# Performance work log

Measured on AMD Instinct MI355X. Metric: run time of the kernel, lower is better.

The kernel has to match this reference:

```python
import jax, jax.numpy as jnp
import numpy as np

N = 512       # num_nodes (feature dim of x == num_nodes, per GCNConv(num_nodes, f1))
BZ = 32       # subjects
TC = 256      # tc_length
F1 = 256
F2 = 128
E = 524288    # edges in the given (corr) graph over all bz*N nodes
NTOT = BZ * N
SLOPE = 0.2   # leaky relu negative_slope


def setup_inputs() -> dict:
    key = jax.random.key(0)
    ks = jax.random.split(key, 17)
    w = lambda k, shape: (jax.random.normal(k, shape, jnp.float32) * (shape[-1] ** -0.5))
    return {
        "x": jax.random.normal(ks[0], (NTOT, N), jnp.float32),
        "t": jax.random.normal(ks[1], (NTOT, TC), jnp.float32),
        "gumbel_u": jax.random.uniform(ks[2], (BZ, N, N, 2), jnp.float32),
        "edge_index": jax.random.randint(ks[3], (2, E), 0, NTOT, jnp.int64 if jax.config.jax_enable_x64 else jnp.int32),
        "conv1_w": w(ks[4], (F1, N)),
        "conv1_b": jnp.zeros((F1,), jnp.float32),
        "conv2_w": w(ks[5], (F2, F1)),
        "conv2_b": jnp.zeros((F2,), jnp.float32),
        "fc_cat_w": w(ks[6], (2, 2 * TC)),
        "fc_cat_b": jnp.zeros((2,), jnp.float32),
        "fcn1_w": w(ks[7], (256, F2 * 2 * N)),
        "fcn1_b": jnp.zeros((256,), jnp.float32),
        "fcn2_w": w(ks[8], (32, 256)),
        "fcn2_b": jnp.zeros((32,), jnp.float32),
        "fcn3_w": w(ks[9], (2, 32)),
        "fcn3_b": jnp.zeros((2,), jnp.float32),
    }


def _gcn_dense(x, A, W, b):
    # PyG GCNConv on a dense 0/1 adjacency A (edge r->c means A[r,c]=1):
    # add self loop, in-degree symmetric norm, aggregate sources into targets.
    n = A.shape[0]
    Ah = A + jnp.eye(n, dtype=A.dtype)
    deg = Ah.sum(axis=0)                                  # in-degree (targets = cols)
    dis = jnp.where(deg > 0, jax.lax.rsqrt(deg), 0.0)
    M = dis[:, None] * Ah * dis[None, :]                  # M[j,i] = d_j^-1/2 A_hat[j,i] d_i^-1/2
    return M.T @ (x @ W.T) + b


def _gcn_sparse(x, row, col, W, b):
    n = x.shape[0]
    loops = jnp.arange(n, dtype=row.dtype)
    r = jnp.concatenate([row, loops])
    c = jnp.concatenate([col, loops])
    deg = jax.ops.segment_sum(jnp.ones_like(c, x.dtype), c, num_segments=n)
    dis = jnp.where(deg > 0, jax.lax.rsqrt(deg), 0.0)
    norm = dis[r] * dis[c]                                # [E+n]
    xw = x @ W.T                                          # [n, out]
    out = jax.ops.segment_sum(xw[r] * norm[:, None], c, num_segments=n)
    return out + b


def reference(x, t, gumbel_u, edge_index, conv1_w, conv1_b, conv2_w, conv2_b,
              fc_cat_w, fc_cat_b, fcn1_w, fcn1_b, fcn2_w, fcn2_b, fcn3_w, fcn3_b):
    bz = t.shape[0] // N
    tb = t.reshape(bz, N, -1)
    xb = x.reshape(bz, N, -1)
    # fc_cat(relu(cat([senders, receivers]))) factors into per-node terms:
    Ws = fc_cat_w[:, :TC]   # multiplies senders half
    Wr = fc_cat_w[:, TC:]   # multiplies receivers half

    def per_sample(ti, xi, ui):
        u = jax.nn.relu(ti)                               # [N, TC]
        ls = u @ Ws.T                                     # [N, 2] sender term
        lr = u @ Wr.T                                     # [N, 2] receiver term
        # pair k = i*N+j has receiver t_i, sender t_j
        logits = lr[:, None, :] + ls[None, :, :] + fc_cat_b   # [N, N, 2]
        g = -jnp.log(-jnp.log(jnp.clip(ui, 1e-9, 1.0 - 1e-9)))  # Gumbel(0,1)
        y = logits + g                                    # tau = 1
        A = (jnp.argmax(y, axis=-1) == 0).astype(xi.dtype)    # hard sample, class 0 => edge
        A = jax.lax.stop_gradient(A)                      # torch.where -> indices blocks grad
        h = jax.nn.relu(_gcn_dense(xi, A, conv1_w, conv1_b))
        return _gcn_dense(h, A, conv2_w, conv2_b)         # [N, F2]

    x_op = jax.vmap(per_sample)(tb, xb, gumbel_u)         # [bz, N, F2]

    row, col = edge_index[0], edge_index[1]
    x_corr = jax.nn.relu(_gcn_sparse(x, row, col, conv1_w, conv1_b))
    x_corr = _gcn_sparse(x_corr, row, col, conv2_w, conv2_b)   # [bz*N, F2]

    emb = jnp.concatenate([x_op.reshape(-1, F2), x_corr], axis=1)  # [bz*N, 2*F2]
    emb = emb.reshape(bz, -1)                             # [bz, 2*F2*N]
    h = jax.nn.leaky_relu(emb @ fcn1_w.T + fcn1_b, SLOPE)
    h = jax.nn.leaky_relu(h @ fcn2_w.T + fcn2_b, SLOPE)
    return h @ fcn3_w.T + fcn3_b                          # [bz, 2]
```

## Files before the change

kernel.cpp:

```cpp
#include <hip/hip_runtime.h>
#include <hip/hip_bf16.h>

typedef __bf16 bf16_t;
typedef __bf16 bf16x8 __attribute__((ext_vector_type(8)));
typedef __bf16 bf16x4 __attribute__((ext_vector_type(4)));
typedef float f32x4 __attribute__((ext_vector_type(4)));

constexpr int kN = 512;
constexpr int kBZ = 32;
constexpr int kTC = 256;
constexpr int kE = 524288;
constexpr int kNTOT = 16384;

__device__ __forceinline__ void gll16(const bf16_t* g, bf16_t* l) {
    __builtin_amdgcn_global_load_lds((const __attribute__((address_space(1))) void*)g,
                                     (__attribute__((address_space(3))) void*)l, 16, 0, 0);
}

template <int NI>
__device__ __forceinline__ void stageT(const bf16_t* __restrict__ src, int ld,
                                       bf16_t* lds, int wave, int lane) {
#pragma unroll
    for (int i = 0; i < NI; i++) {
        int r0 = (wave * NI + i) * 8;
        int r = r0 + (lane >> 3);
        int c = (lane & 7) ^ (r & 7);
        gll16(src + (size_t)r * ld + c * 8, lds + r0 * 64);
    }
}

__device__ __forceinline__ bf16x8 rdfrag(const bf16_t* lds, int row, int cc) {
    return *(const bf16x8*)(lds + row * 64 + ((cc ^ (row & 7)) * 8));
}

__global__ __launch_bounds__(256) void k_front(const float* __restrict__ c1w, const float* __restrict__ c2w,
                                               bf16_t* __restrict__ c1b, bf16_t* __restrict__ c2b,
                                               int* __restrict__ counts, float* __restrict__ degsum,
                                               const float* __restrict__ tin, const float* __restrict__ fcw,
                                               const float* __restrict__ fcb, float4* __restrict__ lsr) {
    int b = blockIdx.x;
    if (b < 192) {
        int i = b * 256 + threadIdx.x;
        const int n0 = 32768, n1 = n0 + 8192, n2 = n1 + 4096, n3 = n2 + 4096;
        if (i < n0) {
            float4 v = ((const float4*)c1w)[i];
            bf16x4 o = {(bf16_t)v.x, (bf16_t)v.y, (bf16_t)v.z, (bf16_t)v.w};
            ((bf16x4*)c1b)[i] = o;
        } else if (i < n1) {
            int j = i - n0;
            float4 v = ((const float4*)c2w)[j];
            bf16x4 o = {(bf16_t)v.x, (bf16_t)v.y, (bf16_t)v.z, (bf16_t)v.w};
            ((bf16x4*)c2b)[j] = o;
        } else if (i < n2) {
            ((int4*)counts)[i - n1] = make_int4(0, 0, 0, 0);
        } else if (i < n3) {
            ((float4*)degsum)[i - n2] = make_float4(0.f, 0.f, 0.f, 0.f);
        }
    } else {
        int row = (b - 192) * 4 + (threadIdx.x >> 6);
        int lane = threadIdx.x & 63;
        const float* tr = tin + (size_t)row * kTC;
        float s0 = 0, s1 = 0, r0 = 0, r1 = 0;
        for (int k = lane; k < kTC; k += 64) {
            float u = fmaxf(tr[k], 0.f);
            s0 += u * fcw[k];
            s1 += u * fcw[512 + k];
            r0 += u * fcw[256 + k];
            r1 += u * fcw[768 + k];
        }
#pragma unroll
        for (int off = 32; off > 0; off >>= 1) {
            s0 += __shfl_down(s0, off); s1 += __shfl_down(s1, off);
            r0 += __shfl_down(r0, off); r1 += __shfl_down(r1, off);
        }
        if (lane == 0) lsr[row] = make_float4(s0 + fcb[0], s1 + fcb[1], r0, r1);
    }
}

__global__ __launch_bounds__(256) void k_adjhist(const float* __restrict__ gum, const float4* __restrict__ lsr,
                                                 bf16_t* __restrict__ AT, float* __restrict__ degsum,
                                                 const int* __restrict__ col, int* __restrict__ counts) {
    int blk = blockIdx.x;
    if (blk >= 2048) {
        int e = (blk - 2048) * 256 + threadIdx.x;
        if (e < kE) atomicAdd(&counts[col[e]], 1);
        return;
    }
    int s = blk >> 6;
    int a0 = ((blk >> 3) & 7) * 64, b0 = (blk & 7) * 64;
    __shared__ bf16_t tile[64][72];
    int t = threadIdx.x;
    int lb = t & 63, ra = t >> 6;
    int b = b0 + lb;
    float4 pb = lsr[s * kN + b];
#pragma unroll 4
    for (int p = 0; p < 16; p++) {
        int a = a0 + p * 4 + ra;
        float4 qa = lsr[s * kN + a];
        float2 gv = *(const float2*)(gum + ((((size_t)s * kN + a) * kN + b) << 1));
        float u0 = fmaxf(gv.x, 1e-9f);
        float u1 = fmaxf(gv.y, 1e-9f);
        float g0 = -__logf(-__logf(u0));
        float g1 = -__logf(-__logf(u1));
        float v = ((qa.z + pb.x + g0) >= (qa.w + pb.y + g1)) ? 1.f : 0.f;
        if (a == b) v += 1.f;
        tile[lb][p * 4 + ra] = (bf16_t)v;
    }
    __syncthreads();
    int rj = t >> 3, li = (t & 7) * 8;
#pragma unroll
    for (int p = 0; p < 2; p++) {
        int j = p * 32 + rj;
        bf16x8 v = *(const bf16x8*)&tile[j][li];
        *(bf16x8*)(AT + ((size_t)s * kN + b0 + j) * kN + a0 + li) = v;
        float ps = 0;
#pragma unroll
        for (int q = 0; q < 8; q++) ps += (float)v[q];
        ps += __shfl_down(ps, 4);
        ps += __shfl_down(ps, 2);
        ps += __shfl_down(ps, 1);
        if ((t & 7) == 0) atomicAdd(degsum + s * kN + b0 + j, ps);
    }
}

template <int MODE, int GDEC>
__global__ __launch_bounds__(256) void k_gemm(const bf16_t* __restrict__ A, const bf16_t* __restrict__ B,
                                              bf16_t* __restrict__ C, int K, int lda, int ldb, int ldc,
                                              size_t sA, size_t sB, size_t sC,
                                              const float* __restrict__ degsum, const float* __restrict__ bias) {
    int m0, n0, s;
    {
        int f = blockIdx.x;
        s = ((f >> 5) << 3) | (f & 7);
        m0 = ((f >> 3) & 3) * 128;
        n0 = 0;
    }
    const bf16_t* Ab = A + sA * s + (size_t)m0 * lda;
    const bf16_t* Bb = B + sB * s + (size_t)n0 * ldb;
    C += sC * s;
    __shared__ __align__(16) bf16_t As[2][128 * 64], Bs[2][128 * 64];
    f32x4 acc[4][4] = {};
    int tid = threadIdx.x;
    int wave = tid >> 6, lane = tid & 63;
    int wm = (wave & 1) * 64, wn = (wave >> 1) * 64;
    int fm = lane & 15, fq = lane >> 4;
    stageT<4>(Ab, lda, As[0], wave, lane);
    stageT<4>(Bb, ldb, Bs[0], wave, lane);
    int cur = 0;
    for (int kb = 0;;) {
        int kn = kb + 64;
        __syncthreads();
        if (kn < K) {
            stageT<4>(Ab + kn, lda, As[cur ^ 1], wave, lane);
            stageT<4>(Bb + kn, ldb, Bs[cur ^ 1], wave, lane);
        }
#pragma unroll
        for (int kk = 0; kk < 2; kk++) {
            bf16x8 af[4], bfr[4];
#pragma unroll
            for (int i = 0; i < 4; i++) {
                af[i] = rdfrag(As[cur], wm + i * 16 + fm, kk * 4 + fq);
                bfr[i] = rdfrag(Bs[cur], wn + i * 16 + fm, kk * 4 + fq);
            }
#pragma unroll
            for (int i = 0; i < 4; i++)
#pragma unroll
                for (int j = 0; j < 4; j++)
                    acc[i][j] = __builtin_amdgcn_mfma_f32_16x16x32_bf16(af[i], bfr[j], acc[i][j], 0, 0, 0);
        }
        kb = kn;
        if (kb >= K) break;
        cur ^= 1;
    }
#pragma unroll
    for (int i = 0; i < 4; i++) {
#pragma unroll
        for (int r = 0; r < 4; r++) {
            int row = wm + i * 16 + fq * 4 + r;
            float sc = rsqrtf(degsum[(size_t)s * kN + m0 + row]);
#pragma unroll
            for (int j = 0; j < 4; j++) {
                int col = n0 + wn + j * 16 + fm;
                float v = sc * acc[i][j][r] + bias[col];
                if constexpr (MODE == 1) v = fmaxf(v, 0.f);
                C[(size_t)(m0 + row) * ldc + col] = (bf16_t)v;
            }
        }
    }
}

__global__ __launch_bounds__(256) void k_gcn1f(const bf16_t* __restrict__ AT, const bf16_t* __restrict__ Z1T,
                                               const bf16_t* __restrict__ C2W, const float* __restrict__ degsum,
                                               const float* __restrict__ c1b, bf16_t* __restrict__ Z2T) {
    int f = blockIdx.x;
    int s = ((f >> 6) << 3) | (f & 7);
    int mt = (f >> 3) & 7;
    const bf16_t* Ab = AT + (size_t)s * (512 * 512) + (size_t)(mt * 64) * 512;
    const bf16_t* Bb = Z1T + (size_t)s * (256 * 512);
    __shared__ __align__(16) bf16_t smem[40960];
    bf16_t* Hs = smem;
    int tid = threadIdx.x, wave = tid >> 6, lane = tid & 63;
    int fm = lane & 15, fq = lane >> 4;
    f32x4 acc[4][4] = {};
    stageT<2>(Ab, 512, smem, wave, lane);
    stageT<8>(Bb, 512, smem + 8192, wave, lane);
    int cur = 0;
    for (int kb = 0;;) {
        int kn = kb + 64;
        bf16_t* Ac = cur ? smem + 4096 : smem;
        bf16_t* An = cur ? smem : smem + 4096;
        bf16_t* Bc = cur ? smem + 24576 : smem + 8192;
        bf16_t* Bn = cur ? smem + 8192 : smem + 24576;
        __syncthreads();
        if (kn < 512) {
            stageT<2>(Ab + kn, 512, An, wave, lane);
            stageT<8>(Bb + kn, 512, Bn, wave, lane);
        }
        int wn = wave * 64;
#pragma unroll
        for (int kk = 0; kk < 2; kk++) {
            bf16x8 af[4], bfr[4];
#pragma unroll
            for (int i = 0; i < 4; i++) {
                af[i] = rdfrag(Ac, i * 16 + fm, kk * 4 + fq);
                bfr[i] = rdfrag(Bc, wn + i * 16 + fm, kk * 4 + fq);
            }
#pragma unroll
            for (int i = 0; i < 4; i++)
#pragma unroll
                for (int j = 0; j < 4; j++)
                    acc[i][j] = __builtin_amdgcn_mfma_f32_16x16x32_bf16(af[i], bfr[j], acc[i][j], 0, 0, 0);
        }
        kb = kn;
        if (kb >= 512) break;
        cur ^= 1;
    }
    __syncthreads();
    stageT<4>(C2W, 256, smem + 16384, wave, lane);
    {
        int wn = wave * 64;
#pragma unroll
        for (int i = 0; i < 4; i++) {
#pragma unroll
            for (int r = 0; r < 4; r++) {
                int row = i * 16 + fq * 4 + r;
                float sc = rsqrtf(degsum[(size_t)s * 512 + mt * 64 + row]);
#pragma unroll
                for (int j = 0; j < 4; j++) {
                    int col = wn + j * 16 + fm;
                    float v = fmaxf(sc * acc[i][j][r] + c1b[col], 0.f);
                    int c = col >> 3;
                    int cS = (c & 24) | ((c & 7) ^ (row & 7));
                    Hs[row * 256 + cS * 8 + (col & 7)] = (bf16_t)v;
                }
            }
        }
    }
    f32x4 acc2[4][2] = {};
    int cur2 = 0;
    for (int kb2 = 0;;) {
        int kn2 = kb2 + 64;
        bf16_t* B2c = cur2 ? smem + 24576 : smem + 16384;
        bf16_t* B2n = cur2 ? smem + 16384 : smem + 24576;
        __syncthreads();
        if (kn2 < 256) stageT<4>(C2W + kn2, 256, B2n, wave, lane);
        int wc = wave * 32;
#pragma unroll
        for (int kk = 0; kk < 2; kk++) {
            int cbase = (kb2 >> 3) + kk * 4 + fq;
            bf16x8 af2[4], bfr2[2];
#pragma unroll
            for (int i = 0; i < 4; i++) {
                int row = i * 16 + fm;
                int cS = (cbase & 24) | ((cbase & 7) ^ (row & 7));
                af2[i] = *(const bf16x8*)&Hs[row * 256 + cS * 8];
            }
#pragma unroll
            for (int j = 0; j < 2; j++) bfr2[j] = rdfrag(B2c, wc + j * 16 + fm, kk * 4 + fq);
#pragma unroll
            for (int i = 0; i < 4; i++)
#pragma unroll
                for (int j = 0; j < 2; j++)
                    acc2[i][j] = __builtin_amdgcn_mfma_f32_16x16x32_bf16(af2[i], bfr2[j], acc2[i][j], 0, 0, 0);
        }
        kb2 = kn2;
        if (kb2 >= 256) break;
        cur2 ^= 1;
    }
    __syncthreads();
    {
        int wc = wave * 32;
#pragma unroll
        for (int i = 0; i < 4; i++) {
#pragma unroll
            for (int r = 0; r < 4; r++) {
                int row = i * 16 + fq * 4 + r;
                float sc = rsqrtf(degsum[(size_t)s * 512 + mt * 64 + row]);
#pragma unroll
                for (int j = 0; j < 2; j++) {
                    int fcol = wc + j * 16 + fm;
                    smem[fcol * 72 + row] = (bf16_t)(sc * acc2[i][j][r]);
                }
            }
        }
    }
    __syncthreads();
    {
        int fr = tid >> 1, half = tid & 1;
        bf16_t* zp = Z2T + ((size_t)(s * 128 + fr)) * 512 + mt * 64 + half * 32;
        const bf16_t* tp = &smem[fr * 72 + half * 32];
#pragma unroll
        for (int q = 0; q < 4; q++) *(bf16x8*)(zp + q * 8) = *(const bf16x8*)(tp + q * 8);
    }
}

template <bool AF32, int F, int DENSE_ROWS, bool PAIRXY>
__global__ __launch_bounds__(256) void k_gemmT(const void* __restrict__ Ap, const bf16_t* __restrict__ B,
                                               bf16_t* __restrict__ XW, bf16_t* __restrict__ ZT, int K,
                                               const float* __restrict__ degsum) {
    int m0, n0;
    if constexpr (PAIRXY) {
        int f = blockIdx.x;
        m0 = (((f >> 4) << 3) | (f & 7)) * 128;
        n0 = ((f >> 3) & 1) * 128;
    } else {
        m0 = blockIdx.x * 128;
        n0 = blockIdx.y * 128;
    }
    constexpr int AST = AF32 ? 9216 : 8192;
    __shared__ __align__(16) bf16_t smem[2 * AST + 2 * 8192];
    bf16_t* A0 = smem;
    bf16_t* A1 = smem + AST;
    bf16_t* B0 = smem + 2 * AST;
    bf16_t* B1 = smem + 2 * AST + 8192;
    f32x4 acc[4][4] = {};
    int tid = threadIdx.x;
    int wave = tid >> 6, lane = tid & 63;
    int wm = (wave & 1) * 64, wn = (wave >> 1) * 64;
    int fm = lane & 15, fq = lane >> 4;
    int srow = tid >> 3, scol = (tid & 7) * 8;
    const float* Af = (const float*)Ap;
    const bf16_t* Abf = (const bf16_t*)Ap;
    if constexpr (AF32) {
#pragma unroll
        for (int p = 0; p < 4; p++) {
            int row = p * 32 + srow;
            const float* ap = Af + (size_t)(m0 + row) * K + scol;
            float4 lo = *(const float4*)ap, hi = *(const float4*)(ap + 4);
            bf16x8 o = {(bf16_t)lo.x, (bf16_t)lo.y, (bf16_t)lo.z, (bf16_t)lo.w,
                        (bf16_t)hi.x, (bf16_t)hi.y, (bf16_t)hi.z, (bf16_t)hi.w};
            *(bf16x8*)&A0[row * 72 + scol] = o;
        }
    } else {
        stageT<4>(Abf + (size_t)m0 * K, K, A0, wave, lane);
    }
    stageT<4>(B + (size_t)n0 * K, K, B0, wave, lane);
    int cur = 0;
    for (int kb = 0;;) {
        int kn = kb + 64;
        bool more = kn < K;
        bf16_t* Ac = cur ? A1 : A0;
        bf16_t* An = cur ? A0 : A1;
        bf16_t* Bc = cur ? B1 : B0;
        bf16_t* Bn = cur ? B0 : B1;
        float4 plo[4], phi[4];
        __syncthreads();
        if (more) {
            if constexpr (AF32) {
#pragma unroll
                for (int p = 0; p < 4; p++) {
                    int row = p * 32 + srow;
                    const float* ap = Af + (size_t)(m0 + row) * K + kn + scol;
                    plo[p] = *(const float4*)ap;
                    phi[p] = *(const float4*)(ap + 4);
                }
            } else {
                stageT<4>(Abf + (size_t)m0 * K + kn, K, An, wave, lane);
            }
            stageT<4>(B + (size_t)n0 * K + kn, K, Bn, wave, lane);
        }
#pragma unroll
        for (int kk = 0; kk < 2; kk++) {
            bf16x8 af[4], bfr[4];
#pragma unroll
            for (int i = 0; i < 4; i++) {
                if constexpr (AF32)
                    af[i] = *(const bf16x8*)&Ac[(wm + i * 16 + fm) * 72 + kk * 32 + fq * 8];
                else
                    af[i] = rdfrag(Ac, wm + i * 16 + fm, kk * 4 + fq);
                bfr[i] = rdfrag(Bc, wn + i * 16 + fm, kk * 4 + fq);
            }
#pragma unroll
            for (int i = 0; i < 4; i++)
#pragma unroll
                for (int j = 0; j < 4; j++)
                    acc[i][j] = __builtin_amdgcn_mfma_f32_16x16x32_bf16(af[i], bfr[j], acc[i][j], 0, 0, 0);
        }
        if constexpr (AF32) {
            if (more) {
#pragma unroll
                for (int p = 0; p < 4; p++) {
                    int row = p * 32 + srow;
                    bf16x8 o = {(bf16_t)plo[p].x, (bf16_t)plo[p].y, (bf16_t)plo[p].z, (bf16_t)plo[p].w,
                                (bf16_t)phi[p].x, (bf16_t)phi[p].y, (bf16_t)phi[p].z, (bf16_t)phi[p].w};
                    *(bf16x8*)&An[row * 72 + scol] = o;
                }
            }
        }
        kb = kn;
        if (kb >= K) break;
        cur ^= 1;
    }
    bool doT = (m0 < DENSE_ROWS);
    __syncthreads();
#pragma unroll
    for (int i = 0; i < 4; i++) {
#pragma unroll
        for (int r = 0; r < 4; r++) {
            int row = wm + i * 16 + fq * 4 + r;
            float sc = doT ? rsqrtf(degsum[m0 + row]) : 0.f;
#pragma unroll
            for (int j = 0; j < 4; j++) {
                int col = wn + j * 16 + fm;
                float v = acc[i][j][r];
                XW[(size_t)(m0 + row) * F + n0 + col] = (bf16_t)v;
                if (doT) smem[col * 136 + row] = (bf16_t)(sc * v);
            }
        }
    }
    if (doT) {
        __syncthreads();
        int fr = tid >> 1, hi = (tid & 1) * 64;
        bf16_t* zrow = ZT + ((size_t)(m0 >> 9) * F + n0 + fr) * kN + (m0 & 511) + hi;
#pragma unroll
        for (int q = 0; q < 8; q++)
            *(bf16x8*)(zrow + q * 8) = *(const bf16x8*)&smem[fr * 136 + hi + q * 8];
    }
}


__global__ __launch_bounds__(1024) void k_scan(const int* __restrict__ counts, int* __restrict__ offsets,
                                               int* __restrict__ cursor, float* __restrict__ dis_s) {
    __shared__ int ldc_[16896];
    __shared__ int sums[1024];
    int t = threadIdx.x;
#define IDX(j) ((j) + ((j) >> 5))
    for (int i = 0; i < 16; i++) {
        int g = i * 1024 + t;
        int c = counts[g];
        ldc_[IDX(g)] = c;
        dis_s[g] = rsqrtf((float)(c + 1));
    }
    __syncthreads();
    int s = 0;
    for (int i = 0; i < 16; i++) s += ldc_[IDX(t * 16 + i)];
    sums[t] = s;
    __syncthreads();
    for (int off = 1; off < 1024; off <<= 1) {
        int y = (t >= off) ? sums[t - off] : 0;
        __syncthreads();
        sums[t] += y;
        __syncthreads();
    }
    int run = sums[t] - s;
    for (int i = 0; i < 16; i++) {
        int j = t * 16 + i;
        int c = ldc_[IDX(j)];
        ldc_[IDX(j)] = run;
        run += c;
    }
    __syncthreads();
    for (int i = 0; i < 16; i++) {
        int g = i * 1024 + t;
        int o = ldc_[IDX(g)];
        offsets[g] = o;
        cursor[g] = o;
    }
#undef IDX
}

__global__ __launch_bounds__(256) void k_fill(const int* __restrict__ row, const int* __restrict__ col,
                                              int* __restrict__ cursor, int* __restrict__ list) {
    int e = blockIdx.x * 256 + threadIdx.x;
    if (e < kE) {
        int p = atomicAdd(&cursor[col[e]], 1);
        list[p] = row[e];
    }
}

template <int F, bool RELU>
__global__ __launch_bounds__(256) void k_sagg(const bf16_t* __restrict__ XW, int rowOffIn,
                                              const int* __restrict__ list, const int* __restrict__ offsets,
                                              const int* __restrict__ counts, const float* __restrict__ dis_s,
                                              const float* __restrict__ bias, bf16_t* __restrict__ OUT,
                                              int outColOff) {
    constexpr int TPR = F / 8;
    constexpr int RPB = 256 / TPR;
    int j = blockIdx.x * RPB + threadIdx.x / TPR;
    int f8 = (threadIdx.x % TPR) * 8;
    float dj = dis_s[j];
    const bf16_t* base = XW + (size_t)rowOffIn * F;
    float acc[8];
    {
        bf16x8 v = *(const bf16x8*)(base + (size_t)j * F + f8);
#pragma unroll
        for (int q = 0; q < 8; q++) acc[q] = dj * (float)v[q];
    }
    int off = offsets[j], cnt = counts[j];
    int e = 0;
    int nb = cnt & ~7;
    if (nb) {
        int r[8];
#pragma unroll
        for (int q = 0; q < 8; q++) r[q] = list[off + q];
        while (true) {
            int en = e + 8;
            bool more = en < nb;
            int rn[8];
            if (more) {
#pragma unroll
                for (int q = 0; q < 8; q++) rn[q] = list[off + en + q];
            }
            float d[8];
#pragma unroll
            for (int q = 0; q < 8; q++) d[q] = dis_s[r[q]];
            bf16x8 v0 = *(const bf16x8*)(base + (size_t)r[0] * F + f8);
            bf16x8 v1 = *(const bf16x8*)(base + (size_t)r[1] * F + f8);
            bf16x8 v2 = *(const bf16x8*)(base + (size_t)r[2] * F + f8);
            bf16x8 v3 = *(const bf16x8*)(base + (size_t)r[3] * F + f8);
            bf16x8 v4 = *(const bf16x8*)(base + (size_t)r[4] * F + f8);
            bf16x8 v5 = *(const bf16x8*)(base + (size_t)r[5] * F + f8);
            bf16x8 v6 = *(const bf16x8*)(base + (size_t)r[6] * F + f8);
            bf16x8 v7 = *(const bf16x8*)(base + (size_t)r[7] * F + f8);
#pragma unroll
            for (int q = 0; q < 8; q++)
                acc[q] += ((d[0] * (float)v0[q] + d[1] * (float)v1[q]) + (d[2] * (float)v2[q] + d[3] * (float)v3[q])) +
                          ((d[4] * (float)v4[q] + d[5] * (float)v5[q]) + (d[6] * (float)v6[q] + d[7] * (float)v7[q]));
            e = en;
            if (!more) break;
#pragma unroll
            for (int q = 0; q < 8; q++) r[q] = rn[q];
        }
    }
    for (; e + 4 <= cnt; e += 4) {
        int r0 = list[off + e], r1 = list[off + e + 1], r2 = list[off + e + 2], r3 = list[off + e + 3];
        float d0 = dis_s[r0], d1 = dis_s[r1], d2 = dis_s[r2], d3 = dis_s[r3];
        bf16x8 v0 = *(const bf16x8*)(base + (size_t)r0 * F + f8);
        bf16x8 v1 = *(const bf16x8*)(base + (size_t)r1 * F + f8);
        bf16x8 v2 = *(const bf16x8*)(base + (size_t)r2 * F + f8);
        bf16x8 v3 = *(const bf16x8*)(base + (size_t)r3 * F + f8);
#pragma unroll
        for (int q = 0; q < 8; q++)
            acc[q] += (d0 * (float)v0[q] + d1 * (float)v1[q]) + (d2 * (float)v2[q] + d3 * (float)v3[q]);
    }
    for (; e < cnt; e++) {
        int r = list[off + e];
        float d = dis_s[r];
        bf16x8 v = *(const bf16x8*)(base + (size_t)r * F + f8);
#pragma unroll
        for (int q = 0; q < 8; q++) acc[q] += d * (float)v[q];
    }
    bf16x8 o;
#pragma unroll
    for (int q = 0; q < 8; q++) {
        float v = dj * acc[q] + bias[f8 + q];
        if (RELU) v = fmaxf(v, 0.f);
        o[q] = (bf16_t)v;
    }
    *(bf16x8*)(OUT + (size_t)j * 256 + outColOff + f8) = o;
}

__global__ __launch_bounds__(256) void k_fcn1(const bf16_t* __restrict__ EMB, const float* __restrict__ W1,
                                              float* __restrict__ partials) {
    int tid = threadIdx.x, wave = tid >> 6, lane = tid & 63;
    int fm = lane & 15, fq = lane >> 4;
    int kb0 = blockIdx.x * 512;
    f32x4 acc[2][4] = {};
#pragma unroll 4
    for (int ks = 0; ks < 512; ks += 32) {
        int k = kb0 + ks + fq * 8;
        bf16x8 a0 = *(const bf16x8*)(EMB + (size_t)fm * 131072 + k);
        bf16x8 a1 = *(const bf16x8*)(EMB + (size_t)(16 + fm) * 131072 + k);
        bf16x8 bfr[4];
#pragma unroll
        for (int j = 0; j < 4; j++) {
            int n = wave * 64 + j * 16 + fm;
            const float* p = W1 + (size_t)n * 131072 + k;
            float4 lo = *(const float4*)p;
            float4 hi = *(const float4*)(p + 4);
            bf16x8 b = {(bf16_t)lo.x, (bf16_t)lo.y, (bf16_t)lo.z, (bf16_t)lo.w,
                        (bf16_t)hi.x, (bf16_t)hi.y, (bf16_t)hi.z, (bf16_t)hi.w};
            bfr[j] = b;
        }
#pragma unroll
        for (int j = 0; j < 4; j++) {
            acc[0][j] = __builtin_amdgcn_mfma_f32_16x16x32_bf16(a0, bfr[j], acc[0][j], 0, 0, 0);
            acc[1][j] = __builtin_amdgcn_mfma_f32_16x16x32_bf16(a1, bfr[j], acc[1][j], 0, 0, 0);
        }
    }
    float* P = partials + (size_t)blockIdx.x * 8192;
#pragma unroll
    for (int i = 0; i < 2; i++)
#pragma unroll
        for (int j = 0; j < 4; j++)
#pragma unroll
            for (int r = 0; r < 4; r++)
                P[(size_t)(i * 16 + fq * 4 + r) * 256 + wave * 64 + j * 16 + fm] = acc[i][j][r];
}

__global__ __launch_bounds__(256) void k_reduce(const float* __restrict__ partials, float* __restrict__ h1pre) {
    __shared__ float red[8][32];
    int t = threadIdx.x;
    int el = t & 31, q = t >> 5;
    int e = blockIdx.x * 32 + el;
    float s = 0;
#pragma unroll 8
    for (int i = 0; i < 32; i++) s += partials[(size_t)(q * 32 + i) * 8192 + e];
    red[q][el] = s;
    __syncthreads();
    if (t < 32) {
        float r = 0;
#pragma unroll
        for (int qq = 0; qq < 8; qq++) r += red[qq][t];
        h1pre[blockIdx.x * 32 + t] = r;
    }
}

__global__ __launch_bounds__(256) void k_head(const float* __restrict__ h1pre, const float* __restrict__ b1,
                                              const float* __restrict__ W2, const float* __restrict__ b2,
                                              const float* __restrict__ W3, const float* __restrict__ b3,
                                              float* __restrict__ out) {
    __shared__ float h1s[32][256];
    __shared__ float h2s[32][32];
    int t = threadIdx.x;
    for (int i = 0; i < 32; i++) {
        float s = h1pre[i * 256 + t] + b1[t];
        h1s[i][t] = (s > 0.f) ? s : 0.2f * s;
    }
    __syncthreads();
    for (int p = 0; p < 4; p++) {
        int id = p * 256 + t, si = id >> 5, o2 = id & 31;
        float s = 0;
        for (int k = 0; k < 256; k++) s += h1s[si][k] * W2[o2 * 256 + k];
        s += b2[o2];
        h2s[si][o2] = (s > 0.f) ? s : 0.2f * s;
    }
    __syncthreads();
    if (t < 64) {
        int si = t >> 1, o3 = t & 1;
        float s = 0;
#pragma unroll
        for (int k = 0; k < 32; k++) s += h2s[si][k] * W3[o3 * 32 + k];
        out[si * 2 + o3] = s + b3[o3];
    }
}


extern "C" void kernel_launch(void* const* d_in, const int* in_sizes, int n_in,
                              void* d_out, int out_size, void* d_ws, size_t ws_size,
                              hipStream_t stream) {
    const float* x = (const float*)d_in[0];
    const float* t = (const float*)d_in[1];
    const float* gum = (const float*)d_in[2];
    const int* eidx = (const int*)d_in[3];
    const float* c1w = (const float*)d_in[4];
    const float* c1b = (const float*)d_in[5];
    const float* c2w = (const float*)d_in[6];
    const float* c2b = (const float*)d_in[7];
    const float* fcw = (const float*)d_in[8];
    const float* fcb = (const float*)d_in[9];
    const float* w1 = (const float*)d_in[10];
    const float* b1 = (const float*)d_in[11];
    const float* w2 = (const float*)d_in[12];
    const float* b2 = (const float*)d_in[13];
    const float* w3 = (const float*)d_in[14];
    const float* b3 = (const float*)d_in[15];
    float* out = (float*)d_out;
    (void)in_sizes; (void)n_in; (void)out_size; (void)ws_size;

    char* ws = (char*)d_ws;
    size_t off = 0;
    auto alloc = [&](size_t bytes) -> char* {
        char* p = ws + off;
        off += (bytes + 255) & ~size_t(255);
        return p;
    };
    bf16_t* c1wb = (bf16_t*)alloc((size_t)256 * 512 * 2);
    bf16_t* c2wb = (bf16_t*)alloc((size_t)128 * 256 * 2);
    float4* lsr = (float4*)alloc((size_t)kNTOT * 16);
    bf16_t* AT = (bf16_t*)alloc((size_t)kBZ * kN * kN * 2);
    float* degsum = (float*)alloc((size_t)kNTOT * 4);
    bf16_t* XW1_EMB = (bf16_t*)alloc((size_t)kNTOT * 256 * 2);
    bf16_t* Z1T = (bf16_t*)alloc((size_t)kBZ * 256 * 512 * 2);
    bf16_t* H = (bf16_t*)alloc((size_t)32768 * 256 * 2);
    bf16_t* XW2 = (bf16_t*)alloc((size_t)32768 * 128 * 2);
    bf16_t* Z2T = (bf16_t*)alloc((size_t)kBZ * 128 * 512 * 2);
    int* counts = (int*)alloc((size_t)kNTOT * 4);
    int* offsets = (int*)alloc((size_t)kNTOT * 4);
    int* cursor = (int*)alloc((size_t)kNTOT * 4);
    float* diss = (float*)alloc((size_t)kNTOT * 4);
    int* list = (int*)alloc((size_t)kE * 4);
    float* partials = (float*)alloc((size_t)256 * 8192 * 4);
    float* h1pre = (float*)alloc((size_t)8192 * 4);

    bf16_t* XW1 = XW1_EMB;
    bf16_t* EMB = XW1_EMB;

    k_front<<<4288, 256, 0, stream>>>(c1w, c2w, c1wb, c2wb, counts, degsum, t, fcw, fcb, lsr);
    k_adjhist<<<4096, 256, 0, stream>>>(gum, lsr, AT, degsum, eidx + kE, counts);
    k_scan<<<1, 1024, 0, stream>>>(counts, offsets, cursor, diss);
    k_fill<<<2048, 256, 0, stream>>>(eidx, eidx + kE, cursor, list);
    k_gemmT<true, 256, kNTOT, true><<<256, 256, 0, stream>>>(x, c1wb, XW1, Z1T, 512, degsum);
    k_gcn1f<<<256, 256, 0, stream>>>(AT, Z1T, c2wb, degsum, c1b, Z2T);
    k_sagg<256, true><<<2048, 256, 0, stream>>>(XW1, 0, list, offsets, counts, diss, c1b,
                                                H + (size_t)16384 * 256, 0);
    k_gemmT<false, 128, 0, false><<<dim3(128, 1, 1), 256, 0, stream>>>(H + (size_t)16384 * 256, c2wb,
                                                                       XW2 + (size_t)16384 * 128, Z2T, 256, degsum);
    k_gemm<2, 2><<<128, 256, 0, stream>>>(AT, Z2T, EMB, 512, 512, 512, 256,
                                          (size_t)512 * 512, (size_t)128 * 512, (size_t)512 * 256,
                                          degsum, c2b);
    k_sagg<128, false><<<1024, 256, 0, stream>>>(XW2, 16384, list, offsets, counts, diss, c2b, EMB, 128);
    k_fcn1<<<256, 256, 0, stream>>>(EMB, w1, partials);
    k_reduce<<<256, 256, 0, stream>>>(partials, h1pre);
    k_head<<<1, 256, 0, stream>>>(h1pre, b1, w2, b2, w3, b3, out);
}
```

Baseline: 482.4 us.

## Bit-pack dense adjacency and unpack in GEMM loops; atomically reduce fcn1 partials

The per-subject dense adjacency is now stored as one bit per entry (u64 words) instead of a bf16 matrix. The two dense GCN aggregation GEMMs expand these bits into bf16 tiles in LDS, adding the self-loop diagonal on the fly, and degsum is initialised to one for the self loop. This cuts adjacency write and read traffic by a factor of sixteen, at the cost of ALU unpacking inside the GEMM loop. Separately, fcn1 now accumulates directly into h1pre with float atomics, which removes the partials buffer and the reduce kernel but makes the summation order nondeterministic.

```diff
diff --git a/kernel.cpp b/kernel.cpp
--- a/kernel.cpp
+++ b/kernel.cpp
@@ -5,6 +5,7 @@
 typedef __bf16 bf16x8 __attribute__((ext_vector_type(8)));
 typedef __bf16 bf16x4 __attribute__((ext_vector_type(4)));
 typedef float f32x4 __attribute__((ext_vector_type(4)));
+typedef unsigned long long u64;
 
 constexpr int kN = 512;
 constexpr int kBZ = 32;
@@ -33,15 +34,33 @@
     return *(const bf16x8*)(lds + row * 64 + ((cc ^ (row & 7)) * 8));
 }
 
+__device__ __forceinline__ void unpackA(bf16_t* lds, int row, int seg2, unsigned bits16, int diagRel) {
+    bf16x8 f0, f1;
+#pragma unroll
+    for (int q = 0; q < 8; q++) f0[q] = ((bits16 >> q) & 1) ? (bf16_t)1.f : (bf16_t)0.f;
+#pragma unroll
+    for (int q = 0; q < 8; q++) f1[q] = ((bits16 >> (8 + q)) & 1) ? (bf16_t)1.f : (bf16_t)0.f;
+    int cc0 = seg2 * 2;
+    *(bf16x8*)(lds + row * 64 + ((cc0 ^ (row & 7)) * 8)) = f0;
+    *(bf16x8*)(lds + row * 64 + (((cc0 + 1) ^ (row & 7)) * 8)) = f1;
+    int rel = diagRel - seg2 * 16;
+    if (rel >= 0 && rel < 16) {
+        int cc = cc0 + (rel >> 3);
+        float base = (float)((bits16 >> rel) & 1);
+        lds[row * 64 + ((cc ^ (row & 7)) * 8) + (rel & 7)] = (bf16_t)(base + 1.f);
+    }
+}
+
 __global__ __launch_bounds__(256) void k_front(const float* __restrict__ c1w, const float* __restrict__ c2w,
                                                bf16_t* __restrict__ c1b, bf16_t* __restrict__ c2b,
                                                int* __restrict__ counts, float* __restrict__ degsum,
+                                               float* __restrict__ h1pre,
                                                const float* __restrict__ tin, const float* __restrict__ fcw,
                                                const float* __restrict__ fcb, float4* __restrict__ lsr) {
     int b = blockIdx.x;
-    if (b < 192) {
+    if (b < 200) {
         int i = b * 256 + threadIdx.x;
-        const int n0 = 32768, n1 = n0 + 8192, n2 = n1 + 4096, n3 = n2 + 4096;
+        const int n0 = 32768, n1 = n0 + 8192, n2 = n1 + 4096, n3 = n2 + 4096, n4 = n3 + 2048;
         if (i < n0) {
             float4 v = ((const float4*)c1w)[i];
             bf16x4 o = {(bf16_t)v.x, (bf16_t)v.y, (bf16_t)v.z, (bf16_t)v.w};
@@ -54,10 +73,12 @@
         } else if (i < n2) {
             ((int4*)counts)[i - n1] = make_int4(0, 0, 0, 0);
         } else if (i < n3) {
-            ((float4*)degsum)[i - n2] = make_float4(0.f, 0.f, 0.f, 0.f);
+            ((float4*)degsum)[i - n2] = make_float4(1.f, 1.f, 1.f, 1.f);
+        } else if (i < n4) {
+            ((float4*)h1pre)[i - n3] = make_float4(0.f, 0.f, 0.f, 0.f);
         }
     } else {
-        int row = (b - 192) * 4 + (threadIdx.x >> 6);
+        int row = (b - 200) * 4 + (threadIdx.x >> 6);
         int lane = threadIdx.x & 63;
         const float* tr = tin + (size_t)row * kTC;
         float s0 = 0, s1 = 0, r0 = 0, r1 = 0;
@@ -78,7 +99,7 @@
 }
 
 __global__ __launch_bounds__(256) void k_adjhist(const float* __restrict__ gum, const float4* __restrict__ lsr,
-                                                 bf16_t* __restrict__ AT, float* __restrict__ degsum,
+                                                 u64* __restrict__ ATb, float* __restrict__ degsum,
                                                  const int* __restrict__ col, int* __restrict__ counts) {
     int blk = blockIdx.x;
     if (blk >= 2048) {
@@ -89,6 +110,7 @@
     int s = blk >> 6;
     int a0 = ((blk >> 3) & 7) * 64, b0 = (blk & 7) * 64;
     __shared__ bf16_t tile[64][72];
+    __shared__ __align__(8) unsigned char bmask[64][8];
     int t = threadIdx.x;
     int lb = t & 63, ra = t >> 6;
     int b = b0 + lb;
@@ -103,117 +125,59 @@
         float g0 = -__logf(-__logf(u0));
         float g1 = -__logf(-__logf(u1));
         float v = ((qa.z + pb.x + g0) >= (qa.w + pb.y + g1)) ? 1.f : 0.f;
-        if (a == b) v += 1.f;
         tile[lb][p * 4 + ra] = (bf16_t)v;
     }
     __syncthreads();
-    int rj = t >> 3, li = (t & 7) * 8;
+    int rj = t >> 3, li8 = t & 7;
 #pragma unroll
     for (int p = 0; p < 2; p++) {
         int j = p * 32 + rj;
-        bf16x8 v = *(const bf16x8*)&tile[j][li];
-        *(bf16x8*)(AT + ((size_t)s * kN + b0 + j) * kN + a0 + li) = v;
-        float ps = 0;
-#pragma unroll
-        for (int q = 0; q < 8; q++) ps += (float)v[q];
-        ps += __shfl_down(ps, 4);
-        ps += __shfl_down(ps, 2);
-        ps += __shfl_down(ps, 1);
-        if ((t & 7) == 0) atomicAdd(degsum + s * kN + b0 + j, ps);
-    }
-}
-
-template <int MODE, int GDEC>
-__global__ __launch_bounds__(256) void k_gemm(const bf16_t* __restrict__ A, const bf16_t* __restrict__ B,
-                                              bf16_t* __restrict__ C, int K, int lda, int ldb, int ldc,
-                                              size_t sA, size_t sB, size_t sC,
-                                              const float* __restrict__ degsum, const float* __restrict__ bias) {
-    int m0, n0, s;
-    {
-        int f = blockIdx.x;
-        s = ((f >> 5) << 3) | (f & 7);
-        m0 = ((f >> 3) & 3) * 128;
-        n0 = 0;
-    }
-    const bf16_t* Ab = A + sA * s + (size_t)m0 * lda;
-    const bf16_t* Bb = B + sB * s + (size_t)n0 * ldb;
-    C += sC * s;
-    __shared__ __align__(16) bf16_t As[2][128 * 64], Bs[2][128 * 64];
-    f32x4 acc[4][4] = {};
-    int tid = threadIdx.x;
-    int wave = tid >> 6, lane = tid & 63;
-    int wm = (wave & 1) * 64, wn = (wave >> 1) * 64;
-    int fm = lane & 15, fq = lane >> 4;
-    stageT<4>(Ab, lda, As[0], wave, lane);
-    stageT<4>(Bb, ldb, Bs[0], wave, lane);
-    int cur = 0;
-    for (int kb = 0;;) {
-        int kn = kb + 64;
-        __syncthreads();
-        if (kn < K) {
-            stageT<4>(Ab + kn, lda, As[cur ^ 1], wave, lane);
-            stageT<4>(Bb + kn, ldb, Bs[cur ^ 1], wave, lane);
-        }
-#pragma unroll
-        for (int kk = 0; kk < 2; kk++) {
-            bf16x8 af[4], bfr[4];
-#pragma unroll
-            for (int i = 0; i < 4; i++) {
-                af[i] = rdfrag(As[cur], wm + i * 16 + fm, kk * 4 + fq);
-                bfr[i] = rdfrag(Bs[cur], wn + i * 16 + fm, kk * 4 + fq);
-            }
-#pragma unroll
-            for (int i = 0; i < 4; i++)
-#pragma unroll
-                for (int j = 0; j < 4; j++)
-                    acc[i][j] = __builtin_amdgcn_mfma_f32_16x16x32_bf16(af[i], bfr[j], acc[i][j], 0, 0, 0);
-        }
-        kb = kn;
-        if (kb >= K) break;
-        cur ^= 1;
-    }
-#pragma unroll
-    for (int i = 0; i < 4; i++) {
-#pragma unroll
-        for (int r = 0; r < 4; r++) {
-            int row = wm + i * 16 + fq * 4 + r;
-            float sc = rsqrtf(degsum[(size_t)s * kN + m0 + row]);
-#pragma unroll
-            for (int j = 0; j < 4; j++) {
-                int col = n0 + wn + j * 16 + fm;
-                float v = sc * acc[i][j][r] + bias[col];
-                if constexpr (MODE == 1) v = fmaxf(v, 0.f);
-                C[(size_t)(m0 + row) * ldc + col] = (bf16_t)v;
-            }
-        }
-    }
-}
-
-__global__ __launch_bounds__(256) void k_gcn1f(const bf16_t* __restrict__ AT, const bf16_t* __restrict__ Z1T,
+        bf16x8 v = *(const bf16x8*)&tile[j][li8 * 8];
+        unsigned b8 = 0;
+#pragma unroll
+        for (int q = 0; q < 8; q++) b8 |= (((float)v[q] != 0.f) ? 1u : 0u) << q;
+        bmask[j][li8] = (unsigned char)b8;
+    }
+    __syncthreads();
+    if (t < 64) {
+        u64 m = *(const u64*)(&bmask[t][0]);
+        ATb[((size_t)s * kN + b0 + t) * 8 + (a0 >> 6)] = m;
+        atomicAdd(degsum + s * kN + b0 + t, (float)__popcll(m));
+    }
+}
+
+__global__ __launch_bounds__(256) void k_gcn1f(const u64* __restrict__ ATb, const bf16_t* __restrict__ Z1T,
                                                const bf16_t* __restrict__ C2W, const float* __restrict__ degsum,
                                                const float* __restrict__ c1b, bf16_t* __restrict__ Z2T) {
     int f = blockIdx.x;
     int s = ((f >> 6) << 3) | (f & 7);
     int mt = (f >> 3) & 7;
-    const bf16_t* Ab = AT + (size_t)s * (512 * 512) + (size_t)(mt * 64) * 512;
     const bf16_t* Bb = Z1T + (size_t)s * (256 * 512);
     __shared__ __align__(16) bf16_t smem[40960];
     bf16_t* Hs = smem;
     int tid = threadIdx.x, wave = tid >> 6, lane = tid & 63;
     int fm = lane & 15, fq = lane >> 4;
     f32x4 acc[4][4] = {};
-    stageT<2>(Ab, 512, smem, wave, lane);
+    int ar = tid & 63, aseg = tid >> 6;
+    int grow = mt * 64 + ar;
+    const u64* aw = ATb + ((size_t)s * kN + grow) * 8;
+    {
+        u64 w0 = aw[0];
+        unpackA(smem, ar, aseg, (unsigned)((w0 >> (aseg * 16)) & 0xFFFFull), grow - 0);
+    }
     stageT<8>(Bb, 512, smem + 8192, wave, lane);
     int cur = 0;
     for (int kb = 0;;) {
         int kn = kb + 64;
+        bool more = kn < 512;
         bf16_t* Ac = cur ? smem + 4096 : smem;
         bf16_t* An = cur ? smem : smem + 4096;
         bf16_t* Bc = cur ? smem + 24576 : smem + 8192;
         bf16_t* Bn = cur ? smem + 8192 : smem + 24576;
+        u64 wn_ = 0;
         __syncthreads();
-        if (kn < 512) {
-            stageT<2>(Ab + kn, 512, An, wave, lane);
+        if (more) {
+            wn_ = aw[kn >> 6];
             stageT<8>(Bb + kn, 512, Bn, wave, lane);
         }
         int wn = wave * 64;
@@ -231,8 +195,10 @@
                 for (int j = 0; j < 4; j++)
                     acc[i][j] = __builtin_amdgcn_mfma_f32_16x16x32_bf16(af[i], bfr[j], acc[i][j], 0, 0, 0);
         }
+        if (more)
+            unpackA(An, ar, aseg, (unsigned)((wn_ >> (aseg * 16)) & 0xFFFFull), grow - kn);
         kb = kn;
-        if (kb >= 512) break;
+        if (!more) break;
         cur ^= 1;
     }
     __syncthreads();
@@ -311,6 +277,76 @@
         const bf16_t* tp = &smem[fr * 72 + half * 32];
 #pragma unroll
         for (int q = 0; q < 4; q++) *(bf16x8*)(zp + q * 8) = *(const bf16x8*)(tp + q * 8);
+    }
+}
+
+__global__ __launch_bounds__(256) void k_gcn2(const u64* __restrict__ ATb, const bf16_t* __restrict__ Z2T,
+                                              bf16_t* __restrict__ EMB, const float* __restrict__ degsum,
+                                              const float* __restrict__ c2b) {
+    int f = blockIdx.x;
+    int s = ((f >> 5) << 3) | (f & 7);
+    int m0 = ((f >> 3) & 3) * 128;
+    const bf16_t* Bb = Z2T + (size_t)s * (128 * 512);
+    __shared__ __align__(16) bf16_t As[2][8192], Bs[2][8192];
+    f32x4 acc[4][4] = {};
+    int tid = threadIdx.x, wave = tid >> 6, lane = tid & 63;
+    int wm = (wave & 1) * 64, wn = (wave >> 1) * 64;
+    int fm = lane & 15, fq = lane >> 4;
+    int ar = tid & 127, aseg = tid >> 7;
+    int grow = m0 + ar;
+    const u64* aw = ATb + ((size_t)s * kN + grow) * 8;
+    {
+        u64 w0 = aw[0];
+        unpackA(As[0], ar, aseg * 2, (unsigned)((w0 >> (aseg * 32)) & 0xFFFFull), grow - 0);
+        unpackA(As[0], ar, aseg * 2 + 1, (unsigned)((w0 >> (aseg * 32 + 16)) & 0xFFFFull), grow - 0);
+    }
+    stageT<4>(Bb, 512, Bs[0], wave, lane);
+    int cur = 0;
+    for (int kb = 0;;) {
+        int kn = kb + 64;
+        bool more = kn < 512;
+        u64 wn_ = 0;
+        __syncthreads();
+        if (more) {
+            wn_ = aw[kn >> 6];
+            stageT<4>(Bb + kn, 512, Bs[cur ^ 1], wave, lane);
+        }
+#pragma unroll
+        for (int kk = 0; kk < 2; kk++) {
+            bf16x8 af[4], bfr[4];
+#pragma unroll
+            for (int i = 0; i < 4; i++) {
+                af[i] = rdfrag(As[cur], wm + i * 16 + fm, kk * 4 + fq);
+                bfr[i] = rdfrag(Bs[cur], wn + i * 16 + fm, kk * 4 + fq);
+            }
+#pragma unroll
+            for (int i = 0; i < 4; i++)
+#pragma unroll
+                for (int j = 0; j < 4; j++)
+                    acc[i][j] = __builtin_amdgcn_mfma_f32_16x16x32_bf16(af[i], bfr[j], acc[i][j], 0, 0, 0);
+        }
+        if (more) {
+            unpackA(As[cur ^ 1], ar, aseg * 2, (unsigned)((wn_ >> (aseg * 32)) & 0xFFFFull), grow - kn);
+            unpackA(As[cur ^ 1], ar, aseg * 2 + 1, (unsigned)((wn_ >> (aseg * 32 + 16)) & 0xFFFFull), grow - kn);
+        }
+        kb = kn;
+        if (!more) break;
+        cur ^= 1;
+    }
+    bf16_t* C = EMB + (size_t)s * (512 * 256);
+#pragma unroll
+    for (int i = 0; i < 4; i++) {
+#pragma unroll
+        for (int r = 0; r < 4; r++) {
+            int row = wm + i * 16 + fq * 4 + r;
+            float sc = rsqrtf(degsum[(size_t)s * kN + m0 + row]);
+#pragma unroll
+            for (int j = 0; j < 4; j++) {
+                int col = wn + j * 16 + fm;
+                float v = sc * acc[i][j][r] + c2b[col];
+                C[(size_t)(m0 + row) * 256 + col] = (bf16_t)v;
+            }
+        }
     }
 }
 
@@ -571,7 +607,7 @@
 }
 
 __global__ __launch_bounds__(256) void k_fcn1(const bf16_t* __restrict__ EMB, const float* __restrict__ W1,
-                                              float* __restrict__ partials) {
+                                              float* __restrict__ h1pre) {
     int tid = threadIdx.x, wave = tid >> 6, lane = tid & 63;
     int fm = lane & 15, fq = lane >> 4;
     int kb0 = blockIdx.x * 512;
@@ -598,32 +634,14 @@
             acc[1][j] = __builtin_amdgcn_mfma_f32_16x16x32_bf16(a1, bfr[j], acc[1][j], 0, 0, 0);
         }
     }
-    float* P = partials + (size_t)blockIdx.x * 8192;
 #pragma unroll
     for (int i = 0; i < 2; i++)
 #pragma unroll
         for (int j = 0; j < 4; j++)
 #pragma unroll
             for (int r = 0; r < 4; r++)
-                P[(size_t)(i * 16 + fq * 4 + r) * 256 + wave * 64 + j * 16 + fm] = acc[i][j][r];
-}
-
-__global__ __launch_bounds__(256) void k_reduce(const float* __restrict__ partials, float* __restrict__ h1pre) {
-    __shared__ float red[8][32];
-    int t = threadIdx.x;
-    int el = t & 31, q = t >> 5;
-    int e = blockIdx.x * 32 + el;
-    float s = 0;
-#pragma unroll 8
-    for (int i = 0; i < 32; i++) s += partials[(size_t)(q * 32 + i) * 8192 + e];
-    red[q][el] = s;
-    __syncthreads();
-    if (t < 32) {
-        float r = 0;
-#pragma unroll
-        for (int qq = 0; qq < 8; qq++) r += red[qq][t];
-        h1pre[blockIdx.x * 32 + t] = r;
-    }
+                atomicAdd(&h1pre[(size_t)(i * 16 + fq * 4 + r) * 256 + wave * 64 + j * 16 + fm],
+                          acc[i][j][r]);
 }
 
 __global__ __launch_bounds__(256) void k_head(const float* __restrict__ h1pre, const float* __restrict__ b1,
@@ -688,7 +706,7 @@
     bf16_t* c1wb = (bf16_t*)alloc((size_t)256 * 512 * 2);
     bf16_t* c2wb = (bf16_t*)alloc((size_t)128 * 256 * 2);
     float4* lsr = (float4*)alloc((size_t)kNTOT * 16);
-    bf16_t* AT = (bf16_t*)alloc((size_t)kBZ * kN * kN * 2);
+    u64* ATb = (u64*)alloc((size_t)kBZ * kN * 8 * 8);
     float* degsum = (float*)alloc((size_t)kNTOT * 4);
     bf16_t* XW1_EMB = (bf16_t*)alloc((size_t)kNTOT * 256 * 2);
     bf16_t* Z1T = (bf16_t*)alloc((size_t)kBZ * 256 * 512 * 2);
@@ -700,27 +718,23 @@
     int* cursor = (int*)alloc((size_t)kNTOT * 4);
     float* diss = (float*)alloc((size_t)kNTOT * 4);
     int* list = (int*)alloc((size_t)kE * 4);
-    float* partials = (float*)alloc((size_t)256 * 8192 * 4);
     float* h1pre = (float*)alloc((size_t)8192 * 4);
 
     bf16_t* XW1 = XW1_EMB;
     bf16_t* EMB = XW1_EMB;
 
-    k_front<<<4288, 256, 0, stream>>>(c1w, c2w, c1wb, c2wb, counts, degsum, t, fcw, fcb, lsr);
-    k_adjhist<<<4096, 256, 0, stream>>>(gum, lsr, AT, degsum, eidx + kE, counts);
+    k_front<<<4296, 256, 0, stream>>>(c1w, c2w, c1wb, c2wb, counts, degsum, h1pre, t, fcw, fcb, lsr);
+    k_adjhist<<<4096, 256, 0, stream>>>(gum, lsr, ATb, degsum, eidx + kE, counts);
     k_scan<<<1, 1024, 0, stream>>>(counts, offsets, cursor, diss);
     k_fill<<<2048, 256, 0, stream>>>(eidx, eidx + kE, cursor, list);
     k_gemmT<true, 256, kNTOT, true><<<256, 256, 0, stream>>>(x, c1wb, XW1, Z1T, 512, degsum);
-    k_gcn1f<<<256, 256, 0, stream>>>(AT, Z1T, c2wb, degsum, c1b, Z2T);
+    k_gcn1f<<<256, 256, 0, stream>>>(ATb, Z1T, c2wb, degsum, c1b, Z2T);
     k_sagg<256, true><<<2048, 256, 0, stream>>>(XW1, 0, list, offsets, counts, diss, c1b,
                                                 H + (size_t)16384 * 256, 0);
     k_gemmT<false, 128, 0, false><<<dim3(128, 1, 1), 256, 0, stream>>>(H + (size_t)16384 * 256, c2wb,
                                                                        XW2 + (size_t)16384 * 128, Z2T, 256, degsum);
-    k_gemm<2, 2><<<128, 256, 0, stream>>>(AT, Z2T, EMB, 512, 512, 512, 256,
-                                          (size_t)512 * 512, (size_t)128 * 512, (size_t)512 * 256,
-                                          degsum, c2b);
+    k_gcn2<<<128, 256, 0, stream>>>(ATb, Z2T, EMB, degsum, c2b);
     k_sagg<128, false><<<1024, 256, 0, stream>>>(XW2, 16384, list, offsets, counts, diss, c2b, EMB, 128);
-    k_fcn1<<<256, 256, 0, stream>>>(EMB, w1, partials);
-    k_reduce<<<256, 256, 0, stream>>>(partials, h1pre);
+    k_fcn1<<<256, 256, 0, stream>>>(EMB, w1, h1pre);
     k_head<<<1, 256, 0, stream>>>(h1pre, b1, w2, b2, w3, b3, out);
 }
```

Result: no change. 487.1 us (+1.0%).
